# Kernel tuning notes

Measured on AMD Instinct MI355X. Metric: run time of the kernel, lower is better.

## Reference

```python
import jax, jax.numpy as jnp
import numpy as np

S_DIM = 128            # attention head width s
E_DIM = 1024           # expansion e = 2*hidden
SQRT_S = 128.0 ** 0.5
EPS = 1e-5


def setup_inputs() -> dict:
    key = jax.random.key(0)
    ks = jax.random.split(key, 8)
    B, S, H = 64, 512, 512
    uv_dim = 2 * E_DIM + S_DIM  # 2176
    # xavier-uniform-ish scale for uv weight
    lim = (6.0 / (H + uv_dim)) ** 0.5
    return {
        "x": jax.random.normal(ks[0], (B, S, H), dtype=jnp.float32),
        "ln_g": jnp.ones((1,), dtype=jnp.float32),
        "uv_w": jax.random.uniform(ks[1], (uv_dim, H), minval=-lim, maxval=lim, dtype=jnp.float32),
        "uv_b": jnp.zeros((uv_dim,), dtype=jnp.float32),
        "gamma": jax.random.uniform(ks[2], (2, S_DIM), dtype=jnp.float32),
        "beta": jax.random.uniform(ks[3], (2, S_DIM), dtype=jnp.float32),
        "w_bias": jax.random.uniform(ks[4], (2 * S - 1,), dtype=jnp.float32),
        "o_w": jax.random.normal(ks[5], (H, E_DIM), dtype=jnp.float32) * 0.02,
        "o_b": jnp.zeros((H,), dtype=jnp.float32),
    }


def _rope(x):
    # x: [B, S, 2, s]; rotate along the sequence dim (dim=1)
    S = x.shape[1]
    half = x.shape[-1] // 2
    pos = jnp.arange(S, dtype=jnp.float32)
    # torch: freq_seq = -arange(half)/half; inv_freq = 10000**(-freq_seq)
    inv_freq = 10000.0 ** (jnp.arange(half, dtype=jnp.float32) / half)
    sinus = pos[:, None, None] * inv_freq[None, None, :]  # [S, 1, half]
    sin, cos = jnp.sin(sinus), jnp.cos(sinus)
    x1, x2 = x[..., :half], x[..., half:]
    return jnp.concatenate([x1 * cos - x2 * sin, x2 * cos + x1 * sin], axis=-1)


def reference(x, ln_g, uv_w, uv_b, gamma, beta, w_bias, o_w, o_b):
    B, S, H = x.shape
    # ScaleNorm
    norm = jnp.linalg.norm(x, axis=-1, keepdims=True) * (H ** -0.5)
    xn = x / jnp.maximum(norm, EPS) * ln_g
    # fused uv projection + SiLU
    act = jax.nn.silu(xn @ uv_w.T + uv_b)  # [B, S, 2e+s]
    u = act[..., :E_DIM]
    v = act[..., E_DIM:2 * E_DIM]
    base = act[..., 2 * E_DIM:]                      # [B, S, s]
    base = base[:, :, None, :] * gamma + beta        # [B, S, 2, s]
    base = _rope(base)
    q, k = base[:, :, 0, :], base[:, :, 1, :]
    # scores + relative position bias: bias[i, j] = w[j - i + S - 1]
    qk = jnp.einsum('bsd,btd->bst', q, k)
    idx = jnp.arange(S)[None, :] - jnp.arange(S)[:, None] + (S - 1)
    qk = qk + w_bias[idx]
    # relu2 similarity kernel
    kernel = jnp.square(jax.nn.relu(qk / SQRT_S))    # [B, S, S]
    out = u * jnp.einsum('bst,bte->bse', kernel, v)  # gated attention
    out = out @ o_w.T + o_b
    return out + x  # use_shortcut: hidden == output
```

## Files before the change

### kernel.cpp

```cpp
#include <hip/hip_runtime.h>
#include <math.h>


#define M_TOT   32768
#define S_LEN   512
#define H_DIM   512
#define E_DIMC  1024
#define UV_DIM  2176
#define UV_PAD  2304
#define D_DIM   128

using floatx4  = __attribute__((ext_vector_type(4))) float;
using uintx2   = __attribute__((ext_vector_type(2))) unsigned int;
using uintx4   = __attribute__((ext_vector_type(4))) unsigned int;
using ushortx4 = __attribute__((ext_vector_type(4))) unsigned short;
using short8   = __attribute__((ext_vector_type(8))) short;

#define ASYNC_CP16(gsrc, ldst)                                                  \
    __builtin_amdgcn_global_load_lds(                                           \
        (const __attribute__((address_space(1))) void*)(gsrc),                  \
        (__attribute__((address_space(3))) void*)(ldst), 16, 0, 0)

__device__ __forceinline__ float bf2f(unsigned short h) {
    union { unsigned int u; float f; } c;
    c.u = ((unsigned int)h) << 16;
    return c.f;
}
__device__ __forceinline__ unsigned short f2bf(float f) {
    union { float f; unsigned int u; } c;
    c.f = f;
    unsigned int r = c.u + 0x7fffu + ((c.u >> 16) & 1u);
    return (unsigned short)(r >> 16);
}
__device__ __forceinline__ float silu_fast(float x) {
    float e = __expf(-x);
    return x * __builtin_amdgcn_rcpf(1.0f + e);
}
__device__ __forceinline__ int xcd_remap(int b, int nwg) {
    return (b & 7) * (nwg >> 3) + (b >> 3);
}

__global__ __launch_bounds__(256) void f2bf_kernel(const float* __restrict__ in,
                                                   unsigned short* __restrict__ out,
                                                   int n4) {
    int i = blockIdx.x * 256 + threadIdx.x;
    if (i < n4) {
        floatx4 v = ((const floatx4*)in)[i];
        ushortx4 o;
        o.x = f2bf(v.x); o.y = f2bf(v.y); o.z = f2bf(v.z); o.w = f2bf(v.w);
        ((ushortx4*)out)[i] = o;
    }
}

__global__ __launch_bounds__(256) void f2bf_pad_kernel(const float* __restrict__ in,
                                                       unsigned short* __restrict__ out,
                                                       int n4_src, int n4_dst) {
    int i = blockIdx.x * 256 + threadIdx.x;
    if (i < n4_dst) {
        ushortx4 o;
        if (i < n4_src) {
            floatx4 v = ((const floatx4*)in)[i];
            o.x = f2bf(v.x); o.y = f2bf(v.y); o.z = f2bf(v.z); o.w = f2bf(v.w);
        } else {
            o.x = 0; o.y = 0; o.z = 0; o.w = 0;
        }
        ((ushortx4*)out)[i] = o;
    }
}

__global__ __launch_bounds__(256) void rmsnorm_kernel(const float* __restrict__ x,
                                                      const float* __restrict__ ln_g,
                                                      unsigned short* __restrict__ xn) {
    int row  = blockIdx.x * 4 + (threadIdx.x >> 6);
    int lane = threadIdx.x & 63;
    const float* xr = x + (size_t)row * H_DIM;
    floatx4 v0 = ((const floatx4*)xr)[lane];
    floatx4 v1 = ((const floatx4*)xr)[lane + 64];
    float ss = v0.x*v0.x + v0.y*v0.y + v0.z*v0.z + v0.w*v0.w
             + v1.x*v1.x + v1.y*v1.y + v1.z*v1.z + v1.w*v1.w;
    #pragma unroll
    for (int off = 32; off > 0; off >>= 1) ss += __shfl_xor(ss, off, 64);
    float norm = sqrtf(ss) * 0.044194173824159216f;
    float sc   = ln_g[0] / fmaxf(norm, 1e-5f);
    unsigned short* xo = xn + (size_t)row * H_DIM;
    ushortx4 o0, o1;
    o0.x = f2bf(v0.x * sc); o0.y = f2bf(v0.y * sc);
    o0.z = f2bf(v0.z * sc); o0.w = f2bf(v0.w * sc);
    o1.x = f2bf(v1.x * sc); o1.y = f2bf(v1.y * sc);
    o1.z = f2bf(v1.z * sc); o1.w = f2bf(v1.w * sc);
    ((ushortx4*)xo)[lane]      = o0;
    ((ushortx4*)xo)[lane + 64] = o1;
}

__global__ __launch_bounds__(64) void rope_table_kernel(float* __restrict__ cost,
                                                        float* __restrict__ sint) {
    int s = blockIdx.x;
    int j = threadIdx.x;
    float invf = (float)pow(10000.0, (double)j / 64.0);
    float ang  = (float)s * invf;
    double a   = (double)ang;
    cost[s * 64 + j] = (float)cos(a);
    sint[s * 64 + j] = (float)sin(a);
}

__global__ __launch_bounds__(256) void rope_apply_kernel(const float* __restrict__ base,
                                                         const float* __restrict__ gamma,
                                                         const float* __restrict__ beta,
                                                         const float* __restrict__ cost,
                                                         const float* __restrict__ sint,
                                                         unsigned short* __restrict__ q,
                                                         unsigned short* __restrict__ k) {
    int idx = blockIdx.x * 256 + threadIdx.x;
    int m = idx >> 6;
    int j = idx & 63;
    int s = m & (S_LEN - 1);
    float b1 = base[(size_t)m * D_DIM + j];
    float b2 = base[(size_t)m * D_DIM + 64 + j];
    float c  = cost[s * 64 + j];
    float sn = sint[s * 64 + j];
    float yq1 = b1 * gamma[j]       + beta[j];
    float yq2 = b2 * gamma[64 + j]  + beta[64 + j];
    float yk1 = b1 * gamma[128 + j] + beta[128 + j];
    float yk2 = b2 * gamma[192 + j] + beta[192 + j];
    q[(size_t)m * D_DIM + j]      = f2bf(yq1 * c - yq2 * sn);
    q[(size_t)m * D_DIM + 64 + j] = f2bf(yq2 * c + yq1 * sn);
    k[(size_t)m * D_DIM + j]      = f2bf(yk1 * c - yk2 * sn);
    k[(size_t)m * D_DIM + 64 + j] = f2bf(yk2 * c + yk1 * sn);
}

template <bool SWAPT>
__device__ __forceinline__ void gemm128_core(const unsigned short* __restrict__ A,
                                             const unsigned short* __restrict__ B,
                                             int lda, int ldb, int K,
                                             int m0, int n0,
                                             unsigned short (&st)[3][12288],
                                             floatx4 (&acc)[4][4]) {
    const int tid  = threadIdx.x;
    const int lane = tid & 63;
    const int wave = tid >> 6;
    const int quad = lane >> 4;
    const int l16  = lane & 15;
    const int wrow = (wave >> 2) * 64;
    const int wcol = (wave & 3) * 64;

    const int qa  = wave * 64 + lane;
    const int Ra  = qa >> 3;
    const int ca  = (qa & 7) ^ (Ra & 7);
    const int srA = 2 * Ra + (ca >> 2);
    const int scA = (ca & 3) * 8;
    const unsigned short* pa  = A + (size_t)(m0 + srA) * lda + scA;
    const unsigned short* pb0 = B + (size_t)(n0 + srA) * ldb + scA;
    const unsigned short* pb1 = pb0 + (size_t)128 * ldb;
    const int ldsA  = (wave * 64) * 8;
    const int ldsB0 = 4096 + (wave * 64) * 8;
    const int ldsB1 = 4096 + (512 + wave * 64) * 8;

    #pragma unroll
    for (int i = 0; i < 4; i++)
        #pragma unroll
        for (int j = 0; j < 4; j++) acc[i][j] = (floatx4){0.f, 0.f, 0.f, 0.f};

    const int NT = K >> 5;
    auto stage = [&](int buf, int t) {
        unsigned short* s = &st[buf][0];
        const int kt = t * 32;
        ASYNC_CP16(pa  + kt, s + ldsA);
        ASYNC_CP16(pb0 + kt, s + ldsB0);
        ASYNC_CP16(pb1 + kt, s + ldsB1);
    };
    stage(0, 0);
    stage(1, 1);

    int aoff[4], boff[4];
    #pragma unroll
    for (int mt = 0; mt < 4; mt++) {
        int r  = wrow + mt * 16 + l16;
        int Rr = r >> 1;
        int cp = (((r & 1) << 2) + quad) ^ (Rr & 7);
        aoff[mt] = Rr * 64 + cp * 8;
    }
    #pragma unroll
    for (int nt = 0; nt < 4; nt++) {
        int r  = wcol + nt * 16 + l16;
        int Rr = r >> 1;
        int cp = (((r & 1) << 2) + quad) ^ (Rr & 7);
        boff[nt] = 4096 + Rr * 64 + cp * 8;
    }

    int bc = 0, bs = 2;
    for (int t = 0; t < NT; ++t) {
        if (t < NT - 1) asm volatile("s_waitcnt vmcnt(3)" ::: "memory");
        else            asm volatile("s_waitcnt vmcnt(0)" ::: "memory");
        __builtin_amdgcn_sched_barrier(0);
        __builtin_amdgcn_s_barrier();
        __builtin_amdgcn_sched_barrier(0);
        if (t + 2 < NT) stage(bs, t + 2);

        const unsigned short* sb = &st[bc][0];
        short8 af[4], bf[4];
        #pragma unroll
        for (int mt = 0; mt < 4; mt++) {
            union { short8 s8; uintx4 u4; } fu;
            fu.u4 = *(const uintx4*)&sb[aoff[mt]];
            af[mt] = fu.s8;
        }
        #pragma unroll
        for (int nt = 0; nt < 4; nt++) {
            union { short8 s8; uintx4 u4; } fu;
            fu.u4 = *(const uintx4*)&sb[boff[nt]];
            bf[nt] = fu.s8;
        }
        __builtin_amdgcn_s_setprio(1);
        #pragma unroll
        for (int mt = 0; mt < 4; mt++)
            #pragma unroll
            for (int nt = 0; nt < 4; nt++)
                acc[mt][nt] = SWAPT
                    ? __builtin_amdgcn_mfma_f32_16x16x32_bf16(bf[nt], af[mt], acc[mt][nt], 0, 0, 0)
                    : __builtin_amdgcn_mfma_f32_16x16x32_bf16(af[mt], bf[nt], acc[mt][nt], 0, 0, 0);
        __builtin_amdgcn_s_setprio(0);

        bc = (bc == 2) ? 0 : bc + 1;
        bs = (bs == 2) ? 0 : bs + 1;
    }
}

union __align__(16) Lds3 {
    unsigned short st[3][12288];
    unsigned short T[128 * 256];
};

__global__ __launch_bounds__(512, 2) void gemm1_128_kernel(const unsigned short* __restrict__ xn,
                                                           const unsigned short* __restrict__ uvw,
                                                           const float* __restrict__ uvb,
                                                           unsigned short* __restrict__ u,
                                                           unsigned short* __restrict__ vT,
                                                           float* __restrict__ base) {
    __shared__ Lds3 lds;
    floatx4 acc[4][4];
    const int bl = blockIdx.y * 9 + blockIdx.x;
    const int lg = xcd_remap(bl, 9 * (M_TOT / 128));
    const int xb = lg % 9;
    const int m0 = (lg / 9) * 128;
    const int tid = threadIdx.x, lane = tid & 63, wave = tid >> 6;
    const int quad = lane >> 4, l16 = lane & 15;
    const int wrow = (wave >> 2) * 64, wcol = (wave & 3) * 64;

    if (xb < 4) {
        const int n0 = xb * 256;
        gemm128_core<true>(xn, uvw, H_DIM, H_DIM, H_DIM, m0, n0, lds.st, acc);
        __syncthreads();
        #pragma unroll
        for (int mt = 0; mt < 4; mt++) {
            int row = wrow + mt * 16 + l16;
            #pragma unroll
            for (int nt = 0; nt < 4; nt++) {
                int nl = wcol + nt * 16 + quad * 4;
                floatx4 b4 = *(const floatx4*)&uvb[n0 + nl];
                ushortx4 pk;
                #pragma unroll
                for (int r = 0; r < 4; r++)
                    pk[r] = f2bf(silu_fast(acc[mt][nt][r] + b4[r]));
                *(uintx2*)&lds.T[row * 256 + (((nl >> 3) ^ (row & 15)) << 3) + (nl & 7)] = *(uintx2*)&pk;
            }
        }
        __syncthreads();
        #pragma unroll
        for (int i = 0; i < 8; i++) {
            int idx = tid + i * 512;
            int row = idx >> 5, c16 = idx & 31;
            *(uintx4*)(u + (size_t)(m0 + row) * E_DIMC + n0 + c16 * 8) =
                *(const uintx4*)&lds.T[row * 256 + ((c16 ^ (row & 15)) << 3)];
        }
    } else if (xb < 8) {
        const int n0 = xb * 256;
        gemm128_core<false>(xn, uvw, H_DIM, H_DIM, H_DIM, m0, n0, lds.st, acc);
        __syncthreads();
        #pragma unroll
        for (int nt = 0; nt < 4; nt++) {
            int rowT = wcol + nt * 16 + l16;
            float bias = uvb[n0 + rowT];
            #pragma unroll
            for (int mt = 0; mt < 4; mt++) {
                int colT = wrow + mt * 16 + quad * 4;
                ushortx4 pk;
                #pragma unroll
                for (int r = 0; r < 4; r++)
                    pk[r] = f2bf(silu_fast(acc[mt][nt][r] + bias));
                *(uintx2*)&lds.T[rowT * 128 + (((colT >> 3) ^ (rowT & 15)) << 3) + (colT & 7)] = *(uintx2*)&pk;
            }
        }
        __syncthreads();
        const int b = m0 >> 9, sg0 = m0 & (S_LEN - 1), eg0 = n0 - E_DIMC;
        #pragma unroll
        for (int i = 0; i < 8; i++) {
            int idx = tid + i * 512;
            int e = idx >> 4, j = idx & 15;
            *(uintx4*)(vT + ((size_t)b * E_DIMC + eg0 + e) * S_LEN + sg0 + j * 8) =
                *(const uintx4*)&lds.T[e * 128 + ((j ^ (e & 15)) << 3)];
        }
    } else {
        const int n0 = 2048;
        gemm128_core<false>(xn, uvw, H_DIM, H_DIM, H_DIM, m0, n0, lds.st, acc);
        if ((wave & 3) < 2) {
            #pragma unroll
            for (int mt = 0; mt < 4; mt++) {
                int m = m0 + wrow + mt * 16 + quad * 4;
                #pragma unroll
                for (int nt = 0; nt < 4; nt++) {
                    int n = wcol + nt * 16 + l16;
                    float bias = uvb[2048 + n];
                    #pragma unroll
                    for (int r = 0; r < 4; r++)
                        base[(size_t)(m + r) * D_DIM + n] = silu_fast(acc[mt][nt][r] + bias);
                }
            }
        }
    }
}

template <bool SWAPT>
__device__ __forceinline__ void gemm256_core(const unsigned short* __restrict__ A,
                                             const unsigned short* __restrict__ B,
                                             int lda, int ldb, int K,
                                             int m0, int n0,
                                             unsigned short (&st)[4][2][128][64],
                                             floatx4 (&acc)[8][4]) {
    const int tid  = threadIdx.x;
    const int lane = tid & 63;
    const int wave = tid >> 6;
    const int quad = lane >> 4;
    const int l16  = lane & 15;
    const int wrow = (wave >> 2) * 128;
    const int wcol = (wave & 3) * 64;

    const int q0    = wave * 128 + lane;
    const int R0    = q0 >> 3;
    const int cp0   = q0 & 7;
    const int c0    = cp0 ^ (R0 & 7);
    const int srow0 = 2 * R0 + (c0 >> 2);
    const int scol0 = (c0 & 3) * 8;

    const unsigned short* pa0 = A + (size_t)(m0 + srow0) * lda + scol0;
    const unsigned short* pa1 = pa0 + (size_t)16 * lda;
    const unsigned short* pb0 = B + (size_t)(n0 + srow0) * ldb + scol0;
    const unsigned short* pb1 = pb0 + (size_t)16 * ldb;
    const int ldsOff0 = (wave * 128) * 8;
    const int ldsOff1 = (wave * 128 + 64) * 8;

    #pragma unroll
    for (int i = 0; i < 8; i++)
        #pragma unroll
        for (int j = 0; j < 4; j++) acc[i][j] = (floatx4){0.f, 0.f, 0.f, 0.f};

    const int NT = K >> 5;
    auto stage = [&](int t) {
        unsigned short* sA = &st[t & 3][0][0][0];
        unsigned short* sB = &st[t & 3][1][0][0];
        const int kt = t * 32;
        ASYNC_CP16(pa0 + kt, sA + ldsOff0);
        ASYNC_CP16(pa1 + kt, sA + ldsOff1);
        ASYNC_CP16(pb0 + kt, sB + ldsOff0);
        ASYNC_CP16(pb1 + kt, sB + ldsOff1);
    };
    stage(0);
    stage(1);
    stage(2);

    int aoff[8], boff[4];
    #pragma unroll
    for (int mt = 0; mt < 8; mt++) {
        int r  = wrow + mt * 16 + l16;
        int Rr = r >> 1;
        int cp = (((r & 1) << 2) + quad) ^ (Rr & 7);
        aoff[mt] = Rr * 64 + cp * 8;
    }
    #pragma unroll
    for (int nt = 0; nt < 4; nt++) {
        int r  = wcol + nt * 16 + l16;
        int Rr = r >> 1;
        int cp = (((r & 1) << 2) + quad) ^ (Rr & 7);
        boff[nt] = Rr * 64 + cp * 8;
    }

    for (int t = 0; t < NT; ++t) {
        if (t < NT - 2)       asm volatile("s_waitcnt vmcnt(8)" ::: "memory");
        else if (t == NT - 2) asm volatile("s_waitcnt vmcnt(4)" ::: "memory");
        else                  asm volatile("s_waitcnt vmcnt(0)" ::: "memory");
        __builtin_amdgcn_sched_barrier(0);
        __builtin_amdgcn_s_barrier();
        __builtin_amdgcn_sched_barrier(0);
        if (t + 3 < NT) stage(t + 3);

        const unsigned short* sA = &st[t & 3][0][0][0];
        const unsigned short* sB = &st[t & 3][1][0][0];
        short8 bf[4];
        #pragma unroll
        for (int nt = 0; nt < 4; nt++) {
            union { short8 s8; uintx4 u4; } fu;
            fu.u4 = *(const uintx4*)&sB[boff[nt]];
            bf[nt] = fu.s8;
        }
        #pragma unroll
        for (int half = 0; half < 2; half++) {
            short8 af[4];
            #pragma unroll
            for (int mt = 0; mt < 4; mt++) {
                union { short8 s8; uintx4 u4; } fu;
                fu.u4 = *(const uintx4*)&sA[aoff[half * 4 + mt]];
                af[mt] = fu.s8;
            }
            __builtin_amdgcn_s_setprio(1);
            #pragma unroll
            for (int mt = 0; mt < 4; mt++)
                #pragma unroll
                for (int nt = 0; nt < 4; nt++)
                    acc[half * 4 + mt][nt] = SWAPT
                        ? __builtin_amdgcn_mfma_f32_16x16x32_bf16(bf[nt], af[mt], acc[half * 4 + mt][nt], 0, 0, 0)
                        : __builtin_amdgcn_mfma_f32_16x16x32_bf16(af[mt], bf[nt], acc[half * 4 + mt][nt], 0, 0, 0);
            __builtin_amdgcn_s_setprio(0);
        }
    }
}

__global__ __launch_bounds__(512, 2) void gemm_out256_kernel(const unsigned short* __restrict__ oe,
                                                             const unsigned short* __restrict__ ow,
                                                             const float* __restrict__ ob,
                                                             const float* __restrict__ x,
                                                             float* __restrict__ out) {
    __shared__ __align__(16) unsigned short st[4][2][128][64];
    floatx4 acc[8][4];
    const int bl = blockIdx.y * 2 + blockIdx.x;
    const int lg = xcd_remap(bl, 2 * (M_TOT / 256));
    const int n0 = (lg & 1) * 256;
    const int m0 = (lg >> 1) * 256;
    gemm256_core<true>(oe, ow, E_DIMC, E_DIMC, E_DIMC, m0, n0, st, acc);

    const int tid = threadIdx.x, lane = tid & 63, wave = tid >> 6;
    const int quad = lane >> 4, l16 = lane & 15;
    const int wrow = (wave >> 2) * 128, wcol = (wave & 3) * 64;
    #pragma unroll
    for (int mt = 0; mt < 8; mt++) {
        int m = m0 + wrow + mt * 16 + l16;
        #pragma unroll
        for (int nt = 0; nt < 4; nt++) {
            int n = n0 + wcol + nt * 16 + quad * 4;
            size_t off = (size_t)m * H_DIM + n;
            floatx4 b4 = *(const floatx4*)&ob[n];
            floatx4 x4 = *(const floatx4*)&x[off];
            *(floatx4*)&out[off] = acc[mt][nt] + b4 + x4;
        }
    }
}

struct GemmLds {
    unsigned short As[128 * 64];
    unsigned short Bs[128 * 64];
};

template <bool SWAPT>
__device__ __forceinline__ void gemm_bt_core(const unsigned short* __restrict__ A,
                                             const unsigned short* __restrict__ B,
                                             int lda, int ldb, int K,
                                             int m0, int n0,
                                             GemmLds& lds, floatx4 (&acc)[4][4]) {
    const int tid  = threadIdx.x;
    const int lane = tid & 63;
    const int wave = tid >> 6;
    const int quad = lane >> 4;
    const int l16  = lane & 15;
    const int wm   = (wave >> 1) * 64;
    const int wn   = (wave & 1) * 64;
    const int lrow = lane >> 3;
    const int cgs  = ((lane & 7) ^ lrow) * 8;

    #pragma unroll
    for (int i = 0; i < 4; i++)
        #pragma unroll
        for (int j = 0; j < 4; j++) acc[i][j] = (floatx4){0.f, 0.f, 0.f, 0.f};

    for (int kt = 0; kt < K; kt += 64) {
        #pragma unroll
        for (int i = 0; i < 4; i++) {
            int r0 = wave * 32 + i * 8;
            const unsigned short* ga = A + (size_t)(m0 + r0 + lrow) * lda + kt + cgs;
            const unsigned short* gb = B + (size_t)(n0 + r0 + lrow) * ldb + kt + cgs;
            ASYNC_CP16(ga, &lds.As[r0 * 64]);
            ASYNC_CP16(gb, &lds.Bs[r0 * 64]);
        }
        __syncthreads();
        #pragma unroll
        for (int kk = 0; kk < 64; kk += 32) {
            short8 af[4], bf[4];
            const int pc = (kk + quad * 8) ^ ((l16 & 7) * 8);
            #pragma unroll
            for (int mt = 0; mt < 4; mt++) {
                int row = wm + mt * 16 + l16;
                union { short8 s8; uintx4 u4; } fu;
                fu.u4 = *(const uintx4*)&lds.As[row * 64 + pc];
                af[mt] = fu.s8;
            }
            #pragma unroll
            for (int nt = 0; nt < 4; nt++) {
                int row = wn + nt * 16 + l16;
                union { short8 s8; uintx4 u4; } fu;
                fu.u4 = *(const uintx4*)&lds.Bs[row * 64 + pc];
                bf[nt] = fu.s8;
            }
            #pragma unroll
            for (int mt = 0; mt < 4; mt++)
                #pragma unroll
                for (int nt = 0; nt < 4; nt++)
                    acc[mt][nt] = SWAPT
                        ? __builtin_amdgcn_mfma_f32_16x16x32_bf16(bf[nt], af[mt], acc[mt][nt], 0, 0, 0)
                        : __builtin_amdgcn_mfma_f32_16x16x32_bf16(af[mt], bf[nt], acc[mt][nt], 0, 0, 0);
        }
        __syncthreads();
    }
}

union LdsU {
    GemmLds g;
    unsigned short T[128 * 128];
};
__device__ __forceinline__ int swz(int row, int col) {
    return row * 128 + ((((col >> 3) ^ (row & 7)) << 3) | (col & 7));
}

__global__ __launch_bounds__(256) void gemm_qk_kernel(const unsigned short* __restrict__ q,
                                                      const unsigned short* __restrict__ k,
                                                      const float* __restrict__ wbias,
                                                      unsigned short* __restrict__ P) {
    __shared__ LdsU lds;
    floatx4 acc[4][4];
    const int bl = (blockIdx.z * 4 + blockIdx.y) * 4 + blockIdx.x;
    const int lg = xcd_remap(bl, 1024);
    const int bx = lg & 3, by = (lg >> 2) & 3, bz = lg >> 4;
    size_t boff = (size_t)bz * S_LEN * D_DIM;
    unsigned short* Pb = P + (size_t)bz * S_LEN * S_LEN;
    const int m0 = bx * 128, n0 = by * 128;
    gemm_bt_core<true>(q + boff, k + boff, D_DIM, D_DIM, D_DIM, m0, n0, lds.g, acc);

    const int tid = threadIdx.x, lane = tid & 63, wave = tid >> 6;
    const int quad = lane >> 4, l16 = lane & 15;
    const int wm = (wave >> 1) * 64, wn = (wave & 1) * 64;
    #pragma unroll
    for (int mt = 0; mt < 4; mt++) {
        int row = wm + mt * 16 + l16;
        int s   = m0 + row;
        #pragma unroll
        for (int nt = 0; nt < 4; nt++) {
            int nl = wn + nt * 16 + quad * 4;
            int t0 = n0 + nl;
            ushortx4 pk;
            #pragma unroll
            for (int r = 0; r < 4; r++) {
                float z = (acc[mt][nt][r] + wbias[t0 + r - s + (S_LEN - 1)]) * 0.08838834764831845f;
                z = fmaxf(z, 0.f);
                pk[r] = f2bf(z * z);
            }
            *(uintx2*)&lds.T[swz(row, nl)] = *(uintx2*)&pk;
        }
    }
    __syncthreads();
    #pragma unroll
    for (int i = 0; i < 8; i++) {
        int idx = tid + i * 256;
        int row = idx >> 4;
        int j   = idx & 15;
        *(uintx4*)(Pb + (size_t)(m0 + row) * S_LEN + n0 + j * 8) =
            *(const uintx4*)&lds.T[swz(row, j * 8)];
    }
}

__global__ __launch_bounds__(256) void gemm_pv_kernel(const unsigned short* __restrict__ P,
                                                      const unsigned short* __restrict__ vT,
                                                      unsigned short* __restrict__ u) {
    __shared__ LdsU lds;
    floatx4 acc[4][4];
    const int bl = (blockIdx.z * 8 + blockIdx.y) * 4 + blockIdx.x;
    const int lg = xcd_remap(bl, 2048);
    const int bx = lg & 3, by = (lg >> 2) & 7, bb = lg >> 5;
    const unsigned short* Pb  = P  + (size_t)bb * S_LEN * S_LEN;
    const unsigned short* vTb = vT + (size_t)bb * E_DIMC * S_LEN;
    const int m0 = bx * 128, n0 = by * 128;
    gemm_bt_core<true>(Pb, vTb, S_LEN, S_LEN, S_LEN, m0, n0, lds.g, acc);

    const int tid = threadIdx.x, lane = tid & 63, wave = tid >> 6;
    const int quad = lane >> 4, l16 = lane & 15;
    const int wm = (wave >> 1) * 64, wn = (wave & 1) * 64;
    #pragma unroll
    for (int mt = 0; mt < 4; mt++) {
        int row = wm + mt * 16 + l16;
        #pragma unroll
        for (int nt = 0; nt < 4; nt++) {
            int nl = wn + nt * 16 + quad * 4;
            ushortx4 pk;
            #pragma unroll
            for (int r = 0; r < 4; r++) pk[r] = f2bf(acc[mt][nt][r]);
            *(uintx2*)&lds.T[swz(row, nl)] = *(uintx2*)&pk;
        }
    }
    __syncthreads();
    #pragma unroll
    for (int i = 0; i < 8; i++) {
        int idx = tid + i * 256;
        int row = idx >> 4;
        int j   = idx & 15;
        size_t off = ((size_t)bb * S_LEN + m0 + row) * E_DIMC + n0 + j * 8;
        union { uintx4 u4; unsigned short s[8]; } tv, uv, ov;
        tv.u4 = *(const uintx4*)&lds.T[swz(row, j * 8)];
        uv.u4 = *(const uintx4*)(u + off);
        #pragma unroll
        for (int jj = 0; jj < 8; jj++) ov.s[jj] = f2bf(bf2f(tv.s[jj]) * bf2f(uv.s[jj]));
        *(uintx4*)(u + off) = ov.u4;
    }
}

extern "C" void kernel_launch(void* const* d_in, const int* in_sizes, int n_in,
                              void* d_out, int out_size, void* d_ws, size_t ws_size,
                              hipStream_t stream) {
    const float* x     = (const float*)d_in[0];
    const float* ln_g  = (const float*)d_in[1];
    const float* uv_w  = (const float*)d_in[2];
    const float* uv_b  = (const float*)d_in[3];
    const float* gamma = (const float*)d_in[4];
    const float* beta  = (const float*)d_in[5];
    const float* wbias = (const float*)d_in[6];
    const float* o_w   = (const float*)d_in[7];
    const float* o_b   = (const float*)d_in[8];
    float* out = (float*)d_out;

    char* ws = (char*)d_ws;
    size_t off = 0;
    auto alloc = [&](size_t bytes) {
        void* p = ws + off;
        off += (bytes + 255) & ~(size_t)255;
        return p;
    };
    unsigned short* u     = (unsigned short*)alloc((size_t)M_TOT * E_DIMC * 2);
    unsigned short* vT    = (unsigned short*)alloc((size_t)64 * E_DIMC * S_LEN * 2);
    unsigned short* xn    = (unsigned short*)alloc((size_t)M_TOT * H_DIM * 2);
    unsigned short* P     = xn;
    float*          base  = (float*)alloc((size_t)M_TOT * D_DIM * 4);
    unsigned short* q     = (unsigned short*)alloc((size_t)M_TOT * D_DIM * 2);
    unsigned short* k     = (unsigned short*)alloc((size_t)M_TOT * D_DIM * 2);
    float*          cost  = (float*)alloc((size_t)S_LEN * 64 * 4);
    float*          sint  = (float*)alloc((size_t)S_LEN * 64 * 4);
    unsigned short* uvwb  = (unsigned short*)alloc((size_t)UV_PAD * H_DIM * 2);
    unsigned short* owb   = (unsigned short*)alloc((size_t)H_DIM * E_DIMC * 2);
    (void)ws_size; (void)in_sizes; (void)n_in; (void)out_size;

    f2bf_pad_kernel<<<(UV_PAD * H_DIM / 4 + 255) / 256, 256, 0, stream>>>(
        uv_w, uvwb, UV_DIM * H_DIM / 4, UV_PAD * H_DIM / 4);
    f2bf_kernel<<<(H_DIM * E_DIMC / 4 + 255) / 256, 256, 0, stream>>>(o_w, owb, H_DIM * E_DIMC / 4);
    rope_table_kernel<<<S_LEN, 64, 0, stream>>>(cost, sint);

    rmsnorm_kernel<<<M_TOT / 4, 256, 0, stream>>>(x, ln_g, xn);

    gemm1_128_kernel<<<dim3(9, M_TOT / 128), 512, 0, stream>>>(xn, uvwb, uv_b, u, vT, base);

    rope_apply_kernel<<<M_TOT * 64 / 256, 256, 0, stream>>>(base, gamma, beta, cost, sint, q, k);

    gemm_qk_kernel<<<dim3(S_LEN / 128, S_LEN / 128, 64), 256, 0, stream>>>(q, k, wbias, P);

    gemm_pv_kernel<<<dim3(S_LEN / 128, E_DIMC / 128, 64), 256, 0, stream>>>(P, vT, u);

    gemm_out256_kernel<<<dim3(H_DIM / 256, M_TOT / 256), 512, 0, stream>>>(u, owb, o_b, x, out);
}
```

Before: 357.6 us.

## Fuse prep kernels into one launch and fold RoPE into gemm1 epilogue

Merges the weight bf16 conversions, the RoPE table build and the row normalisation into a single block-partitioned prep kernel, cutting several launches. The RoPE/gamma/beta application moves into the gemm1 epilogue for the base tile: SiLU outputs are staged in LDS and q/k are written directly. This removes the fp32 base buffer round trip through global memory and the separate rope kernel. The cost is extra LDS use, two barriers and longer epilogue work in those gemm1 blocks.

```diff
diff --git a/kernel.cpp b/kernel.cpp
--- a/kernel.cpp
+++ b/kernel.cpp
@@ -40,92 +40,63 @@
     return (b & 7) * (nwg >> 3) + (b >> 3);
 }
 
-__global__ __launch_bounds__(256) void f2bf_kernel(const float* __restrict__ in,
-                                                   unsigned short* __restrict__ out,
-                                                   int n4) {
-    int i = blockIdx.x * 256 + threadIdx.x;
-    if (i < n4) {
-        floatx4 v = ((const floatx4*)in)[i];
+__global__ __launch_bounds__(256) void prep_kernel(const float* __restrict__ x,
+                                                   const float* __restrict__ ln_g,
+                                                   unsigned short* __restrict__ xn,
+                                                   const float* __restrict__ uv_w,
+                                                   unsigned short* __restrict__ uvwb,
+                                                   const float* __restrict__ o_w,
+                                                   unsigned short* __restrict__ owb,
+                                                   float* __restrict__ cost,
+                                                   float* __restrict__ sint) {
+    const int bid = blockIdx.x;
+    const int tid = threadIdx.x;
+    if (bid < 8192) {
+        int row  = bid * 4 + (tid >> 6);
+        int lane = tid & 63;
+        const float* xr = x + (size_t)row * H_DIM;
+        floatx4 v0 = ((const floatx4*)xr)[lane];
+        floatx4 v1 = ((const floatx4*)xr)[lane + 64];
+        float ss = v0.x*v0.x + v0.y*v0.y + v0.z*v0.z + v0.w*v0.w
+                 + v1.x*v1.x + v1.y*v1.y + v1.z*v1.z + v1.w*v1.w;
+        #pragma unroll
+        for (int off = 32; off > 0; off >>= 1) ss += __shfl_xor(ss, off, 64);
+        float norm = sqrtf(ss) * 0.044194173824159216f;
+        float sc   = ln_g[0] / fmaxf(norm, 1e-5f);
+        unsigned short* xo = xn + (size_t)row * H_DIM;
+        ushortx4 o0, o1;
+        o0.x = f2bf(v0.x * sc); o0.y = f2bf(v0.y * sc);
+        o0.z = f2bf(v0.z * sc); o0.w = f2bf(v0.w * sc);
+        o1.x = f2bf(v1.x * sc); o1.y = f2bf(v1.y * sc);
+        o1.z = f2bf(v1.z * sc); o1.w = f2bf(v1.w * sc);
+        ((ushortx4*)xo)[lane]      = o0;
+        ((ushortx4*)xo)[lane + 64] = o1;
+    } else if (bid < 9344) {
+        int i = (bid - 8192) * 256 + tid;
         ushortx4 o;
-        o.x = f2bf(v.x); o.y = f2bf(v.y); o.z = f2bf(v.z); o.w = f2bf(v.w);
-        ((ushortx4*)out)[i] = o;
-    }
-}
-
-__global__ __launch_bounds__(256) void f2bf_pad_kernel(const float* __restrict__ in,
-                                                       unsigned short* __restrict__ out,
-                                                       int n4_src, int n4_dst) {
-    int i = blockIdx.x * 256 + threadIdx.x;
-    if (i < n4_dst) {
-        ushortx4 o;
-        if (i < n4_src) {
-            floatx4 v = ((const floatx4*)in)[i];
+        if (i < UV_DIM * H_DIM / 4) {
+            floatx4 v = ((const floatx4*)uv_w)[i];
             o.x = f2bf(v.x); o.y = f2bf(v.y); o.z = f2bf(v.z); o.w = f2bf(v.w);
         } else {
             o.x = 0; o.y = 0; o.z = 0; o.w = 0;
         }
-        ((ushortx4*)out)[i] = o;
-    }
-}
-
-__global__ __launch_bounds__(256) void rmsnorm_kernel(const float* __restrict__ x,
-                                                      const float* __restrict__ ln_g,
-                                                      unsigned short* __restrict__ xn) {
-    int row  = blockIdx.x * 4 + (threadIdx.x >> 6);
-    int lane = threadIdx.x & 63;
-    const float* xr = x + (size_t)row * H_DIM;
-    floatx4 v0 = ((const floatx4*)xr)[lane];
-    floatx4 v1 = ((const floatx4*)xr)[lane + 64];
-    float ss = v0.x*v0.x + v0.y*v0.y + v0.z*v0.z + v0.w*v0.w
-             + v1.x*v1.x + v1.y*v1.y + v1.z*v1.z + v1.w*v1.w;
-    #pragma unroll
-    for (int off = 32; off > 0; off >>= 1) ss += __shfl_xor(ss, off, 64);
-    float norm = sqrtf(ss) * 0.044194173824159216f;
-    float sc   = ln_g[0] / fmaxf(norm, 1e-5f);
-    unsigned short* xo = xn + (size_t)row * H_DIM;
-    ushortx4 o0, o1;
-    o0.x = f2bf(v0.x * sc); o0.y = f2bf(v0.y * sc);
-    o0.z = f2bf(v0.z * sc); o0.w = f2bf(v0.w * sc);
-    o1.x = f2bf(v1.x * sc); o1.y = f2bf(v1.y * sc);
-    o1.z = f2bf(v1.z * sc); o1.w = f2bf(v1.w * sc);
-    ((ushortx4*)xo)[lane]      = o0;
-    ((ushortx4*)xo)[lane + 64] = o1;
-}
-
-__global__ __launch_bounds__(64) void rope_table_kernel(float* __restrict__ cost,
-                                                        float* __restrict__ sint) {
-    int s = blockIdx.x;
-    int j = threadIdx.x;
-    float invf = (float)pow(10000.0, (double)j / 64.0);
-    float ang  = (float)s * invf;
-    double a   = (double)ang;
-    cost[s * 64 + j] = (float)cos(a);
-    sint[s * 64 + j] = (float)sin(a);
-}
-
-__global__ __launch_bounds__(256) void rope_apply_kernel(const float* __restrict__ base,
-                                                         const float* __restrict__ gamma,
-                                                         const float* __restrict__ beta,
-                                                         const float* __restrict__ cost,
-                                                         const float* __restrict__ sint,
-                                                         unsigned short* __restrict__ q,
-                                                         unsigned short* __restrict__ k) {
-    int idx = blockIdx.x * 256 + threadIdx.x;
-    int m = idx >> 6;
-    int j = idx & 63;
-    int s = m & (S_LEN - 1);
-    float b1 = base[(size_t)m * D_DIM + j];
-    float b2 = base[(size_t)m * D_DIM + 64 + j];
-    float c  = cost[s * 64 + j];
-    float sn = sint[s * 64 + j];
-    float yq1 = b1 * gamma[j]       + beta[j];
-    float yq2 = b2 * gamma[64 + j]  + beta[64 + j];
-    float yk1 = b1 * gamma[128 + j] + beta[128 + j];
-    float yk2 = b2 * gamma[192 + j] + beta[192 + j];
-    q[(size_t)m * D_DIM + j]      = f2bf(yq1 * c - yq2 * sn);
-    q[(size_t)m * D_DIM + 64 + j] = f2bf(yq2 * c + yq1 * sn);
-    k[(size_t)m * D_DIM + j]      = f2bf(yk1 * c - yk2 * sn);
-    k[(size_t)m * D_DIM + 64 + j] = f2bf(yk2 * c + yk1 * sn);
+        ((ushortx4*)uvwb)[i] = o;
+    } else if (bid < 9856) {
+        int i = (bid - 9344) * 256 + tid;
+        floatx4 v = ((const floatx4*)o_w)[i];
+        ushortx4 o;
+        o.x = f2bf(v.x); o.y = f2bf(v.y); o.z = f2bf(v.z); o.w = f2bf(v.w);
+        ((ushortx4*)owb)[i] = o;
+    } else {
+        int idx = (bid - 9856) * 256 + tid;
+        int s = idx >> 6;
+        int j = idx & 63;
+        float invf = (float)pow(10000.0, (double)j / 64.0);
+        float ang  = (float)s * invf;
+        double a   = (double)ang;
+        cost[s * 64 + j] = (float)cos(a);
+        sint[s * 64 + j] = (float)sin(a);
+    }
 }
 
 template <bool SWAPT>
@@ -228,6 +199,7 @@
 union __align__(16) Lds3 {
     unsigned short st[3][12288];
     unsigned short T[128 * 256];
+    float          Tf[128][132];
 };
 
 __global__ __launch_bounds__(512, 2) void gemm1_128_kernel(const unsigned short* __restrict__ xn,
@@ -235,7 +207,12 @@
                                                            const float* __restrict__ uvb,
                                                            unsigned short* __restrict__ u,
                                                            unsigned short* __restrict__ vT,
-                                                           float* __restrict__ base) {
+                                                           const float* __restrict__ gamma,
+                                                           const float* __restrict__ beta,
+                                                           const float* __restrict__ cost,
+                                                           const float* __restrict__ sint,
+                                                           unsigned short* __restrict__ q,
+                                                           unsigned short* __restrict__ k) {
     __shared__ Lds3 lds;
     floatx4 acc[4][4];
     const int bl = blockIdx.y * 9 + blockIdx.x;
@@ -302,19 +279,40 @@
     } else {
         const int n0 = 2048;
         gemm128_core<false>(xn, uvw, H_DIM, H_DIM, H_DIM, m0, n0, lds.st, acc);
+        __syncthreads();
         if ((wave & 3) < 2) {
             #pragma unroll
             for (int mt = 0; mt < 4; mt++) {
-                int m = m0 + wrow + mt * 16 + quad * 4;
+                int rowl = wrow + mt * 16 + quad * 4;
                 #pragma unroll
                 for (int nt = 0; nt < 4; nt++) {
                     int n = wcol + nt * 16 + l16;
                     float bias = uvb[2048 + n];
                     #pragma unroll
                     for (int r = 0; r < 4; r++)
-                        base[(size_t)(m + r) * D_DIM + n] = silu_fast(acc[mt][nt][r] + bias);
+                        lds.Tf[rowl + r][n] = silu_fast(acc[mt][nt][r] + bias);
                 }
             }
+        }
+        __syncthreads();
+        #pragma unroll
+        for (int i = 0; i < 16; i++) {
+            int idx = tid + i * 512;
+            int row = idx >> 6, j = idx & 63;
+            int s   = (m0 + row) & (S_LEN - 1);
+            float b1 = lds.Tf[row][j];
+            float b2 = lds.Tf[row][j + 64];
+            float c  = cost[s * 64 + j];
+            float sn = sint[s * 64 + j];
+            float yq1 = b1 * gamma[j]       + beta[j];
+            float yq2 = b2 * gamma[64 + j]  + beta[64 + j];
+            float yk1 = b1 * gamma[128 + j] + beta[128 + j];
+            float yk2 = b2 * gamma[192 + j] + beta[192 + j];
+            size_t mo = (size_t)(m0 + row) * D_DIM;
+            q[mo + j]      = f2bf(yq1 * c - yq2 * sn);
+            q[mo + 64 + j] = f2bf(yq2 * c + yq1 * sn);
+            k[mo + j]      = f2bf(yk1 * c - yk2 * sn);
+            k[mo + 64 + j] = f2bf(yk2 * c + yk1 * sn);
         }
     }
 }
@@ -642,7 +640,6 @@
     unsigned short* vT    = (unsigned short*)alloc((size_t)64 * E_DIMC * S_LEN * 2);
     unsigned short* xn    = (unsigned short*)alloc((size_t)M_TOT * H_DIM * 2);
     unsigned short* P     = xn;
-    float*          base  = (float*)alloc((size_t)M_TOT * D_DIM * 4);
     unsigned short* q     = (unsigned short*)alloc((size_t)M_TOT * D_DIM * 2);
     unsigned short* k     = (unsigned short*)alloc((size_t)M_TOT * D_DIM * 2);
     float*          cost  = (float*)alloc((size_t)S_LEN * 64 * 4);
@@ -651,16 +648,10 @@
     unsigned short* owb   = (unsigned short*)alloc((size_t)H_DIM * E_DIMC * 2);
     (void)ws_size; (void)in_sizes; (void)n_in; (void)out_size;
 
-    f2bf_pad_kernel<<<(UV_PAD * H_DIM / 4 + 255) / 256, 256, 0, stream>>>(
-        uv_w, uvwb, UV_DIM * H_DIM / 4, UV_PAD * H_DIM / 4);
-    f2bf_kernel<<<(H_DIM * E_DIMC / 4 + 255) / 256, 256, 0, stream>>>(o_w, owb, H_DIM * E_DIMC / 4);
-    rope_table_kernel<<<S_LEN, 64, 0, stream>>>(cost, sint);
-
-    rmsnorm_kernel<<<M_TOT / 4, 256, 0, stream>>>(x, ln_g, xn);
-
-    gemm1_128_kernel<<<dim3(9, M_TOT / 128), 512, 0, stream>>>(xn, uvwb, uv_b, u, vT, base);
-
-    rope_apply_kernel<<<M_TOT * 64 / 256, 256, 0, stream>>>(base, gamma, beta, cost, sint, q, k);
+    prep_kernel<<<9984, 256, 0, stream>>>(x, ln_g, xn, uv_w, uvwb, o_w, owb, cost, sint);
+
+    gemm1_128_kernel<<<dim3(9, M_TOT / 128), 512, 0, stream>>>(
+        xn, uvwb, uv_b, u, vT, gamma, beta, cost, sint, q, k);
 
     gemm_qk_kernel<<<dim3(S_LEN / 128, S_LEN / 128, 64), 256, 0, stream>>>(q, k, wbias, P);
 
```

New measurement: 354.7 us. About the same (-0.8%).
